# Kernel tuning notes

Measured on AMD Instinct MI355X. Metric: run time of the kernel, lower is better.

Reference implementation:

```python
import jax, jax.numpy as jnp
import numpy as np

# ---- static LSS config (matches init_kwargs) ----
B, N = 4, 6
OGFH, OGFW, DS = 256, 704, 16
FH, FW = OGFH // DS, OGFW // DS            # 16, 44
D_LO, D_HI, D_STEP = 4.0, 45.0, 1.0
D = 41                                      # len(arange(4,45,1))
CAMC = 64
NX, NY, NZ = 200, 200, 1
DX = np.array([0.5, 0.5, 20.0], np.float32)
BX = np.array([-50.0 + 0.25, -50.0 + 0.25, -10.0 + 10.0], np.float32)  # lower + dx/2


def make_frustum():
    ds = jnp.arange(D_LO, D_HI, D_STEP, dtype=jnp.float32)[:, None, None]  # (D,1,1)
    xs = jnp.linspace(0.0, OGFW - 1.0, FW, dtype=jnp.float32)[None, None, :]
    ys = jnp.linspace(0.0, OGFH - 1.0, FH, dtype=jnp.float32)[None, :, None]
    ds, ys, xs = jnp.broadcast_arrays(ds, ys, xs)
    return jnp.stack([xs, ys, ds], axis=-1)  # (D, FH, FW, 3)


def setup_inputs() -> dict:
    key = jax.random.key(0)
    k1, k2 = jax.random.split(key)
    # depthnet output (pre-softmax depth logits + context features)
    x_feats = jax.random.normal(k1, (B, N, D + CAMC, FH, FW), dtype=jnp.float32)
    # cam-to-ego rotation: camera z (depth) -> ego x, so points land in the grid
    R = np.array([[0.0, 0.0, 1.0], [-1.0, 0.0, 0.0], [0.0, -1.0, 0.0]], np.float32)
    rots = jnp.asarray(np.broadcast_to(R, (B, N, 3, 3)).copy())
    trans = jax.random.normal(k2, (B, N, 3), dtype=jnp.float32) * 0.5
    f, cx, cy = 500.0, OGFW / 2.0, OGFH / 2.0
    K = np.array([[f, 0.0, cx], [0.0, f, cy], [0.0, 0.0, 1.0]], np.float32)
    intrins = jnp.asarray(np.broadcast_to(K, (B, N, 3, 3)).copy())
    post_rots = jnp.asarray(np.broadcast_to(np.eye(3, dtype=np.float32), (B, N, 3, 3)).copy())
    post_trans = jnp.zeros((B, N, 3), dtype=jnp.float32)
    return {"x_feats": x_feats, "rots": rots, "trans": trans,
            "intrins": intrins, "post_rots": post_rots, "post_trans": post_trans}


def reference(x_feats, rots, trans, intrins, post_rots, post_trans):
    # ---- lift: depth distribution x context features ----
    depth = jax.nn.softmax(x_feats[:, :, :D], axis=2)           # (B,N,D,h,w)
    feat = x_feats[:, :, D:D + CAMC]                            # (B,N,C,h,w)
    lifted = jnp.einsum('bndhw,bnchw->bndhwc', depth, feat)     # (B,N,D,h,w,C)

    # ---- geometry: per-pixel 3D points in ego frame ----
    frustum = make_frustum()                                    # (D,h,w,3)
    pts = frustum[None, None] - post_trans[:, :, None, None, None, :]
    pts = jnp.einsum('bnij,bndhwj->bndhwi', jnp.linalg.inv(post_rots), pts)
    pts = jnp.concatenate([pts[..., :2] * pts[..., 2:3], pts[..., 2:3]], axis=-1)
    combine = rots @ jnp.linalg.inv(intrins)
    pts = jnp.einsum('bnij,bndhwj->bndhwi', combine, pts) + trans[:, :, None, None, None, :]

    # ---- voxel pooling (scatter-add == bev_pool sum) ----
    dx = jnp.asarray(DX); bx = jnp.asarray(BX)
    gidx = jnp.floor((pts - (bx - dx / 2.0)) / dx).astype(jnp.int32)  # (B,N,D,h,w,3)
    ix, iy, iz = gidx[..., 0], gidx[..., 1], gidx[..., 2]
    valid = (ix >= 0) & (ix < NX) & (iy >= 0) & (iy < NY) & (iz >= 0) & (iz < NZ)
    b_ix = jnp.arange(B, dtype=jnp.int32)[:, None, None, None, None]
    flat = ((b_ix * NZ + iz) * NX + ix) * NY + iy                # (B,N,D,h,w)
    total = B * NZ * NX * NY
    flat = jnp.where(valid, flat, total)                         # invalid -> dump bin
    out = jax.ops.segment_sum(lifted.reshape(-1, CAMC), flat.reshape(-1),
                              num_segments=total + 1)[:total]
    # (B,NZ,NX,NY,C) -> final[b, :, z, x, y], then cat z-slices along channels
    out = out.reshape(B, NZ, NX, NY, CAMC).transpose(0, 1, 4, 2, 3)
    return out.reshape(B, NZ * CAMC, NX, NY)                     # (4, 64, 200, 200)
```

## Files before the change

kernel.cpp:

```cpp
#include <hip/hip_runtime.h>
#include <math.h>

#define BB 4
#define NN 6
#define DD 41
#define CC 64
#define FHh 16
#define FWw 44
#define NXg 200
#define NYg 200
#define NZg 1
#define NPIX (BB*NN*FHh*FWw)
#define NSLOT 256
#define NOVF  (FHh*DD)
#define WSFLOATS (BB*NZg*NXg*NYg*CC)

__device__ __forceinline__ void inv3x3d(const double m[9], double o[9]) {
    double a=m[0],b=m[1],c=m[2],d=m[3],e=m[4],f=m[5],g=m[6],h=m[7],i=m[8];
    double A = e*i - f*h;
    double Bv = -(d*i - f*g);
    double Cv = d*h - e*g;
    double det = a*A + b*Bv + c*Cv;
    double r = 1.0/det;
    o[0]=A*r;  o[1]=-(b*i-c*h)*r; o[2]=(b*f-c*e)*r;
    o[3]=Bv*r; o[4]=(a*i-c*g)*r;  o[5]=-(a*f-c*d)*r;
    o[6]=Cv*r; o[7]=-(a*h-b*g)*r; o[8]=(a*e-b*d)*r;
}

__global__ __launch_bounds__(256)
void lss_zero(float4* __restrict__ p, int n4)
{
    const int stride = gridDim.x * 256;
    for (int i = blockIdx.x * 256 + threadIdx.x; i < n4; i += stride)
        p[i] = make_float4(0.f, 0.f, 0.f, 0.f);
}

__global__ __launch_bounds__(256)
void lss_scatter_dedup(const float* __restrict__ xf,
                       const float* __restrict__ rots,
                       const float* __restrict__ trans,
                       const float* __restrict__ intr,
                       const float* __restrict__ prots,
                       const float* __restrict__ ptrans,
                       float* __restrict__ ws)
{
    __shared__ int   s_keys[NSLOT];
    __shared__ float s_coef[NSLOT * FHh];
    __shared__ float s_feat[FHh * CC];
    __shared__ int2  s_ovf[NOVF];
    __shared__ float s_ovfw[NOVF];
    __shared__ int   s_ovfcnt;

    const int tid  = threadIdx.x;
    const int lane = tid & 63;
    const int wv   = tid >> 6;

    const int bid = blockIdx.x;
    const int w   = bid % FWw;
    const int rem = bid / FWw;
    const int n   = rem % NN;
    const int b   = rem / NN;
    const int cam = b*NN + n;
    const size_t pixoff = (size_t)cam * (DD+CC) * FHh * FWw + w;

    s_keys[tid] = -1;
    #pragma unroll
    for (int i = tid; i < NSLOT*FHh; i += 256) s_coef[i] = 0.0f;
    if (tid == 0) s_ovfcnt = 0;
    #pragma unroll
    for (int i = tid; i < FHh*CC; i += 256) {
        int c = i & 63, h = i >> 6;
        s_feat[i] = xf[pixoff + (size_t)(DD + c) * (FHh*FWw) + h * FWw];
    }

    double K9[9], P9[9], R9[9];
    #pragma unroll
    for (int i = 0; i < 9; ++i) {
        K9[i] = (double)intr [cam*9 + i];
        P9[i] = (double)prots[cam*9 + i];
        R9[i] = (double)rots [cam*9 + i];
    }
    double Kinv[9], Pinv[9];
    inv3x3d(K9, Kinv);
    inv3x3d(P9, Pinv);
    double M[9];
    #pragma unroll
    for (int i = 0; i < 3; ++i)
        #pragma unroll
        for (int j = 0; j < 3; ++j)
            M[i*3+j] = R9[i*3+0]*Kinv[0*3+j] + R9[i*3+1]*Kinv[1*3+j] + R9[i*3+2]*Kinv[2*3+j];
    const double tx  = (double)trans [cam*3+0], ty  = (double)trans [cam*3+1], tz  = (double)trans [cam*3+2];
    const double ptx = (double)ptrans[cam*3+0], pty = (double)ptrans[cam*3+1], ptz = (double)ptrans[cam*3+2];

    __syncthreads();

    for (int r = 0; r < 4; ++r) {
        const int h = (wv << 2) + r;
        float logit = (lane < DD)
            ? xf[pixoff + (size_t)lane * (FHh*FWw) + h * FWw] : -INFINITY;
        float mx = logit;
        #pragma unroll
        for (int off = 32; off; off >>= 1) mx = fmaxf(mx, __shfl_xor(mx, off));
        float ex = (lane < DD) ? expf(logit - mx) : 0.0f;
        float sm = ex;
        #pragma unroll
        for (int off = 32; off; off >>= 1) sm += __shfl_xor(sm, off);
        const float wgt = ex / sm;

        int seg = -1;
        if (lane < DD) {
            double dz = 4.0 + (double)lane;
            double xs = (double)w * (703.0/43.0);
            double ys = (double)h * 17.0;
            double px = xs - ptx, py = ys - pty, pz = dz - ptz;
            double qx = Pinv[0]*px + Pinv[1]*py + Pinv[2]*pz;
            double qy = Pinv[3]*px + Pinv[4]*py + Pinv[5]*pz;
            double qz = Pinv[6]*px + Pinv[7]*py + Pinv[8]*pz;
            qx *= qz; qy *= qz;
            double gx = M[0]*qx + M[1]*qy + M[2]*qz + tx;
            double gy = M[3]*qx + M[4]*qy + M[5]*qz + ty;
            double gz = M[6]*qx + M[7]*qy + M[8]*qz + tz;
            double fx = floor((gx + 50.0) / 0.5);
            double fy = floor((gy + 50.0) / 0.5);
            double fz = floor((gz + 10.0) / 20.0);
            if (fx >= 0.0 && fx < (double)NXg &&
                fy >= 0.0 && fy < (double)NYg &&
                fz >= 0.0 && fz < (double)NZg) {
                int ix = (int)fx, iy = (int)fy, iz = (int)fz;
                seg = ((b*NZg + iz)*NXg + ix)*NYg + iy;
            }
        }

        if (seg >= 0) {
            unsigned slot = (((unsigned)seg * 2654435761u) >> 20) & (NSLOT-1);
            bool done = false;
            for (int probe = 0; probe < NSLOT; ++probe) {
                int prev = atomicCAS(&s_keys[slot], -1, seg);
                if (prev == -1 || prev == seg) {
                    atomicAdd(&s_coef[slot*FHh + h], wgt);
                    done = true;
                    break;
                }
                slot = (slot + 1) & (NSLOT-1);
            }
            if (!done) {
                int k = atomicAdd(&s_ovfcnt, 1);
                s_ovf[k]  = make_int2(seg, h);
                s_ovfw[k] = wgt;
            }
        }
    }

    __syncthreads();

    for (int s = wv; s < NSLOT; s += 4) {
        int key = s_keys[s];
        if (key < 0) continue;
        float acc = 0.0f;
        #pragma unroll
        for (int h = 0; h < FHh; ++h)
            acc += s_coef[s*FHh + h] * s_feat[(h << 6) + lane];
        atomicAdd(&ws[(size_t)key * CC + lane], acc);
    }
    const int novf = s_ovfcnt;
    for (int e = wv; e < novf; e += 4) {
        int seg = s_ovf[e].x, h = s_ovf[e].y;
        atomicAdd(&ws[(size_t)seg * CC + lane], s_ovfw[e] * s_feat[(h << 6) + lane]);
    }
}

__global__ __launch_bounds__(256)
void lss_scatter_direct(const float* __restrict__ xf,
                        const float* __restrict__ rots,
                        const float* __restrict__ trans,
                        const float* __restrict__ intr,
                        const float* __restrict__ prots,
                        const float* __restrict__ ptrans,
                        float* __restrict__ acc)
{
    const int wid  = blockIdx.x * 4 + (threadIdx.x >> 6);
    const int lane = threadIdx.x & 63;
    if (wid >= NPIX) return;
    int w  = wid % FWw;
    int t1 = wid / FWw;
    int h  = t1 % FHh; t1 /= FHh;
    int n  = t1 % NN;
    int b  = t1 / NN;
    const int cam = b*NN + n;

    double K9[9], P9[9], R9[9];
    #pragma unroll
    for (int i = 0; i < 9; ++i) {
        K9[i] = (double)intr [cam*9 + i];
        P9[i] = (double)prots[cam*9 + i];
        R9[i] = (double)rots [cam*9 + i];
    }
    double Kinv[9], Pinv[9];
    inv3x3d(K9, Kinv);
    inv3x3d(P9, Pinv);
    double M[9];
    #pragma unroll
    for (int i = 0; i < 3; ++i)
        #pragma unroll
        for (int j = 0; j < 3; ++j)
            M[i*3+j] = R9[i*3+0]*Kinv[0*3+j] + R9[i*3+1]*Kinv[1*3+j] + R9[i*3+2]*Kinv[2*3+j];
    const double tx  = (double)trans [cam*3+0], ty  = (double)trans [cam*3+1], tz  = (double)trans [cam*3+2];
    const double ptx = (double)ptrans[cam*3+0], pty = (double)ptrans[cam*3+1], ptz = (double)ptrans[cam*3+2];

    const size_t pixoff = (size_t)cam * (DD+CC) * FHh * FWw + (size_t)h * FWw + w;
    float logit = (lane < DD) ? xf[pixoff + (size_t)lane * (FHh*FWw)] : -INFINITY;
    float mx = logit;
    #pragma unroll
    for (int off = 32; off; off >>= 1) mx = fmaxf(mx, __shfl_xor(mx, off));
    float ex = (lane < DD) ? expf(logit - mx) : 0.0f;
    float sm = ex;
    #pragma unroll
    for (int off = 32; off; off >>= 1) sm += __shfl_xor(sm, off);
    const float wgt = ex / sm;

    int baddr = -1;
    if (lane < DD) {
        double dz = 4.0 + (double)lane;
        double xs = (double)w * (703.0/43.0);
        double ys = (double)h * 17.0;
        double px = xs - ptx, py = ys - pty, pz = dz - ptz;
        double qx = Pinv[0]*px + Pinv[1]*py + Pinv[2]*pz;
        double qy = Pinv[3]*px + Pinv[4]*py + Pinv[5]*pz;
        double qz = Pinv[6]*px + Pinv[7]*py + Pinv[8]*pz;
        qx *= qz; qy *= qz;
        double gx = M[0]*qx + M[1]*qy + M[2]*qz + tx;
        double gy = M[3]*qx + M[4]*qy + M[5]*qz + ty;
        double gz = M[6]*qx + M[7]*qy + M[8]*qz + tz;
        double fx = floor((gx + 50.0) / 0.5);
        double fy = floor((gy + 50.0) / 0.5);
        double fz = floor((gz + 10.0) / 20.0);
        if (fx >= 0.0 && fx < (double)NXg &&
            fy >= 0.0 && fy < (double)NYg &&
            fz >= 0.0 && fz < (double)NZg) {
            int ix = (int)fx, iy = (int)fy, iz = (int)fz;
            int bz = b*NZg + iz;
            baddr = bz * (CC*NXg*NYg) + ix*NYg + iy;
        }
    }

    const float f = xf[pixoff + (size_t)(DD + lane) * (FHh*FWw)];
    for (int d = 0; d < DD; ++d) {
        int   a  = __shfl(baddr, d);
        float wd = __shfl(wgt,   d);
        if (a >= 0) atomicAdd(&acc[(size_t)a + (size_t)lane * (NXg*NYg)], wd * f);
    }
}

__global__ __launch_bounds__(256)
void lss_transpose(const float* __restrict__ ws, float* __restrict__ out)
{
    __shared__ float tile[64][65];
    const int blk  = blockIdx.x;
    const int bz   = blk / 625;
    const int xy0  = (blk % 625) * 64;
    const int lane = threadIdx.x & 63;
    const int grp  = threadIdx.x >> 6;

    const float* src = ws + ((size_t)bz * 40000 + xy0) * CC;
    #pragma unroll
    for (int i = 0; i < 16; ++i) {
        int r = grp * 16 + i;
        tile[r][lane] = src[(size_t)r * CC + lane];
    }
    __syncthreads();
    float* dst = out + (size_t)bz * CC * 40000 + xy0;
    #pragma unroll
    for (int i = 0; i < 16; ++i) {
        int cRow = grp * 16 + i;
        dst[(size_t)cRow * 40000 + lane] = tile[lane][cRow];
    }
}

extern "C" void kernel_launch(void* const* d_in, const int* in_sizes, int n_in,
                              void* d_out, int out_size, void* d_ws, size_t ws_size,
                              hipStream_t stream) {
    const float* xf     = (const float*)d_in[0];
    const float* rots   = (const float*)d_in[1];
    const float* trans  = (const float*)d_in[2];
    const float* intr   = (const float*)d_in[3];
    const float* prots  = (const float*)d_in[4];
    const float* ptrans = (const float*)d_in[5];
    float* out = (float*)d_out;

    const size_t need = (size_t)WSFLOATS * sizeof(float);

    if (ws_size >= need) {
        float* ws = (float*)d_ws;
        lss_zero<<<dim3(2048), dim3(256), 0, stream>>>((float4*)ws, WSFLOATS/4);
        lss_scatter_dedup<<<dim3(BB*NN*FWw), dim3(256), 0, stream>>>(
            xf, rots, trans, intr, prots, ptrans, ws);
        lss_transpose<<<dim3(BB*NZg*625), dim3(256), 0, stream>>>(ws, out);
    } else {
        lss_zero<<<dim3(2048), dim3(256), 0, stream>>>((float4*)out, WSFLOATS/4);
        lss_scatter_direct<<<dim3((NPIX + 3) / 4), dim3(256), 0, stream>>>(
            xf, rots, trans, intr, prots, ptrans, out);
    }
}
```

Baseline: 55.44 us.

## Replace atomic scatter into zeroed workspace with per-voxel linked-list gather

The old path zeroed a full 41 MB voxel-by-channel workspace, scatter-added into it with global float atomics, then transposed it into the output. The new path has each column block record its occupied voxels and 16 per-row coefficients into a record buffer, linked per voxel through an atomicExch head array, and saves that column's features. A gather kernel then walks each voxel's list, computes the channel sums, and writes the output directly in channel-major order. This drops the large zero fill, the float atomics and the transpose pass, at the cost of pointer-chasing reads, a smaller hash table with a last-voxel shortcut, and a block-index remap.

Result: slower. 86.72 us (+56.4%).

```diff
diff --git a/kernel.cpp b/kernel.cpp
--- a/kernel.cpp
+++ b/kernel.cpp
@@ -10,10 +10,20 @@
 #define NXg 200
 #define NYg 200
 #define NZg 1
+#define NSLOT 128
+#define NOVF  (FHh*DD)
+#define XYg (NXg*NYg)
+#define NVOX (BB*NZg*NXg*NYg)
+#define NCOL (BB*NN*FWw)
 #define NPIX (BB*NN*FHh*FWw)
-#define NSLOT 256
-#define NOVF  (FHh*DD)
-#define WSFLOATS (BB*NZg*NXg*NYg*CC)
+#define MAXREC (NCOL*NOVF)
+#define RECI 20
+
+#define HEAD_OFF 0
+#define CNT_OFF  (NVOX*4)
+#define REC_OFF  (1u<<20)
+#define FT_OFF   (REC_OFF + MAXREC*RECI*4)
+#define WS_NEED  (FT_OFF + NCOL*FHh*CC*4)
 
 __device__ __forceinline__ void inv3x3d(const double m[9], double o[9]) {
     double a=m[0],b=m[1],c=m[2],d=m[3],e=m[4],f=m[5],g=m[6],h=m[7],i=m[8];
@@ -28,49 +38,51 @@
 }
 
 __global__ __launch_bounds__(256)
-void lss_zero(float4* __restrict__ p, int n4)
+void lss_build(const float* __restrict__ xf,
+               const float* __restrict__ rots,
+               const float* __restrict__ trans,
+               const float* __restrict__ intr,
+               const float* __restrict__ prots,
+               const float* __restrict__ ptrans,
+               int* __restrict__ head,
+               int* __restrict__ cnt,
+               int* __restrict__ recs,
+               float* __restrict__ fT)
 {
-    const int stride = gridDim.x * 256;
-    for (int i = blockIdx.x * 256 + threadIdx.x; i < n4; i += stride)
-        p[i] = make_float4(0.f, 0.f, 0.f, 0.f);
-}
-
-__global__ __launch_bounds__(256)
-void lss_scatter_dedup(const float* __restrict__ xf,
-                       const float* __restrict__ rots,
-                       const float* __restrict__ trans,
-                       const float* __restrict__ intr,
-                       const float* __restrict__ prots,
-                       const float* __restrict__ ptrans,
-                       float* __restrict__ ws)
-{
+    __shared__ float s_lg[FHh * FWw];
+    __shared__ float s_feat[FHh * CC];
+    __shared__ float s_coef[NSLOT * 17];
     __shared__ int   s_keys[NSLOT];
-    __shared__ float s_coef[NSLOT * FHh];
-    __shared__ float s_feat[FHh * CC];
+    __shared__ short s_list[NSLOT];
+    __shared__ int   s_nslot;
     __shared__ int2  s_ovf[NOVF];
     __shared__ float s_ovfw[NOVF];
     __shared__ int   s_ovfcnt;
+    __shared__ int   s_base;
 
     const int tid  = threadIdx.x;
     const int lane = tid & 63;
     const int wv   = tid >> 6;
 
-    const int bid = blockIdx.x;
+    const int obid = blockIdx.x;
+    const int bid  = (obid & 7) * (NCOL / 8) + (obid >> 3);
     const int w   = bid % FWw;
     const int rem = bid / FWw;
     const int n   = rem % NN;
     const int b   = rem / NN;
     const int cam = b*NN + n;
-    const size_t pixoff = (size_t)cam * (DD+CC) * FHh * FWw + w;
-
-    s_keys[tid] = -1;
-    #pragma unroll
-    for (int i = tid; i < NSLOT*FHh; i += 256) s_coef[i] = 0.0f;
-    if (tid == 0) s_ovfcnt = 0;
-    #pragma unroll
-    for (int i = tid; i < FHh*CC; i += 256) {
-        int c = i & 63, h = i >> 6;
-        s_feat[i] = xf[pixoff + (size_t)(DD + c) * (FHh*FWw) + h * FWw];
+    const float* colbase = xf + (size_t)cam * (DD+CC) * FHh * FWw + w;
+
+    if (tid < NSLOT) s_keys[tid] = -1;
+    for (int i = tid; i < NSLOT*17; i += 256) s_coef[i] = 0.0f;
+    if (tid == 0) { s_nslot = 0; s_ovfcnt = 0; }
+
+    for (int t = tid; t < (DD+CC)*FHh; t += 256) {
+        int h  = t / (DD+CC);
+        int ch = t - h*(DD+CC);
+        float v = colbase[(size_t)ch * (FHh*FWw) + h * FWw];
+        if (ch < DD) s_lg[h*FWw + ch] = v;
+        else         s_feat[(h << 6) + (ch - DD)] = v;
     }
 
     double K9[9], P9[9], R9[9];
@@ -94,10 +106,11 @@
 
     __syncthreads();
 
+    int      last_vox  = -1;
+    unsigned last_slot = 0;
     for (int r = 0; r < 4; ++r) {
         const int h = (wv << 2) + r;
-        float logit = (lane < DD)
-            ? xf[pixoff + (size_t)lane * (FHh*FWw) + h * FWw] : -INFINITY;
+        float logit = (lane < DD) ? s_lg[h*FWw + lane] : -INFINITY;
         float mx = logit;
         #pragma unroll
         for (int off = 32; off; off >>= 1) mx = fmaxf(mx, __shfl_xor(mx, off));
@@ -107,7 +120,7 @@
         for (int off = 32; off; off >>= 1) sm += __shfl_xor(sm, off);
         const float wgt = ex / sm;
 
-        int seg = -1;
+        int vox = -1;
         if (lane < DD) {
             double dz = 4.0 + (double)lane;
             double xs = (double)w * (703.0/43.0);
@@ -127,45 +140,121 @@
                 fy >= 0.0 && fy < (double)NYg &&
                 fz >= 0.0 && fz < (double)NZg) {
                 int ix = (int)fx, iy = (int)fy, iz = (int)fz;
-                seg = ((b*NZg + iz)*NXg + ix)*NYg + iy;
+                vox = ((b*NZg + iz)*NXg + ix)*NYg + iy;
             }
         }
 
-        if (seg >= 0) {
-            unsigned slot = (((unsigned)seg * 2654435761u) >> 20) & (NSLOT-1);
-            bool done = false;
-            for (int probe = 0; probe < NSLOT; ++probe) {
-                int prev = atomicCAS(&s_keys[slot], -1, seg);
-                if (prev == -1 || prev == seg) {
-                    atomicAdd(&s_coef[slot*FHh + h], wgt);
-                    done = true;
-                    break;
+        if (vox >= 0) {
+            if (vox == last_vox) {
+                atomicAdd(&s_coef[last_slot*17 + h], wgt);
+            } else {
+                unsigned slot = (((unsigned)vox * 2654435761u) >> 18) & (NSLOT-1);
+                bool done = false;
+                for (int probe = 0; probe < NSLOT; ++probe) {
+                    int prev = atomicCAS(&s_keys[slot], -1, vox);
+                    if (prev == -1) {
+                        int k = atomicAdd(&s_nslot, 1);
+                        s_list[k] = (short)slot;
+                    }
+                    if (prev == -1 || prev == vox) {
+                        atomicAdd(&s_coef[slot*17 + h], wgt);
+                        last_vox = vox; last_slot = slot;
+                        done = true;
+                        break;
+                    }
+                    slot = (slot + 1) & (NSLOT-1);
                 }
-                slot = (slot + 1) & (NSLOT-1);
+                if (!done) {
+                    int k = atomicAdd(&s_ovfcnt, 1);
+                    s_ovf[k]  = make_int2(vox, h);
+                    s_ovfw[k] = wgt;
+                    last_vox = -1;
+                }
             }
-            if (!done) {
-                int k = atomicAdd(&s_ovfcnt, 1);
-                s_ovf[k]  = make_int2(seg, h);
-                s_ovfw[k] = wgt;
-            }
         }
     }
 
     __syncthreads();
 
-    for (int s = wv; s < NSLOT; s += 4) {
-        int key = s_keys[s];
-        if (key < 0) continue;
-        float acc = 0.0f;
-        #pragma unroll
-        for (int h = 0; h < FHh; ++h)
-            acc += s_coef[s*FHh + h] * s_feat[(h << 6) + lane];
-        atomicAdd(&ws[(size_t)key * CC + lane], acc);
-    }
+    const int nocc = s_nslot;
     const int novf = s_ovfcnt;
+    if (tid == 0) s_base = atomicAdd(cnt, nocc + novf);
+    {
+        float* ft = fT + (size_t)bid * (FHh*CC);
+        for (int i = tid; i < FHh*CC; i += 256) ft[i] = s_feat[i];
+    }
+    __syncthreads();
+    const int base = s_base;
+
+    for (int e = wv; e < nocc; e += 4) {
+        int slot = s_list[e];
+        int vox  = s_keys[slot];
+        int ridx = base + e;
+        int* rec = recs + (size_t)ridx * RECI;
+        if (lane >= 32 && lane < 48)
+            ((float*)rec)[4 + (lane-32)] = s_coef[slot*17 + (lane-32)];
+        if (lane == 0) {
+            rec[0] = vox;
+            rec[2] = bid;
+            rec[1] = atomicExch(&head[vox], ridx);
+        }
+    }
     for (int e = wv; e < novf; e += 4) {
-        int seg = s_ovf[e].x, h = s_ovf[e].y;
-        atomicAdd(&ws[(size_t)seg * CC + lane], s_ovfw[e] * s_feat[(h << 6) + lane]);
+        int vox = s_ovf[e].x, h = s_ovf[e].y;
+        int ridx = base + nocc + e;
+        int* rec = recs + (size_t)ridx * RECI;
+        if (lane >= 32 && lane < 48)
+            ((float*)rec)[4 + (lane-32)] = ((lane-32) == h) ? s_ovfw[e] : 0.0f;
+        if (lane == 0) {
+            rec[0] = vox;
+            rec[2] = bid;
+            rec[1] = atomicExch(&head[vox], ridx);
+        }
+    }
+}
+
+__global__ __launch_bounds__(256)
+void lss_gather(const int* __restrict__ head,
+                const int* __restrict__ recs,
+                const float* __restrict__ fT,
+                float* __restrict__ out)
+{
+    __shared__ float s_acc[CC * 65];
+    const int blk  = blockIdx.x;
+    const int bz   = blk / 625;
+    const int xy0  = (blk % 625) * 64;
+    const int tid  = threadIdx.x;
+    const int lane = tid & 63;
+    const int wv   = tid >> 6;
+
+    for (int cell = wv; cell < 64; cell += 4) {
+        const int vox = bz * XYg + xy0 + cell;
+        float a = 0.0f;
+        int ptr = head[vox];
+        while (ptr >= 0) {
+            const int* rec = recs + (size_t)ptr * RECI;
+            const int col  = rec[2];
+            const float4* cp = (const float4*)(rec + 4);
+            float4 c0 = cp[0], c1 = cp[1], c2 = cp[2], c3 = cp[3];
+            const float* fb = fT + (size_t)col * (FHh*CC) + lane;
+            a += c0.x*fb[0*64]  + c0.y*fb[1*64]  + c0.z*fb[2*64]  + c0.w*fb[3*64]
+               + c1.x*fb[4*64]  + c1.y*fb[5*64]  + c1.z*fb[6*64]  + c1.w*fb[7*64]
+               + c2.x*fb[8*64]  + c2.y*fb[9*64]  + c2.z*fb[10*64] + c2.w*fb[11*64]
+               + c3.x*fb[12*64] + c3.y*fb[13*64] + c3.z*fb[14*64] + c3.w*fb[15*64];
+            ptr = rec[1];
+        }
+        s_acc[lane*65 + cell] = a;
+    }
+    __syncthreads();
+
+    float* dst = out + (size_t)bz * CC * XYg + xy0;
+    #pragma unroll
+    for (int rep = 0; rep < 4; ++rep) {
+        int c = (wv << 4) + (rep << 2) + (lane >> 4);
+        int q = lane & 15;
+        float4 v = make_float4(s_acc[c*65 + 4*q + 0], s_acc[c*65 + 4*q + 1],
+                               s_acc[c*65 + 4*q + 2], s_acc[c*65 + 4*q + 3]);
+        ((float4*)(dst + (size_t)c * XYg))[q] = v;
     }
 }
 
@@ -239,7 +328,7 @@
             fz >= 0.0 && fz < (double)NZg) {
             int ix = (int)fx, iy = (int)fy, iz = (int)fz;
             int bz = b*NZg + iz;
-            baddr = bz * (CC*NXg*NYg) + ix*NYg + iy;
+            baddr = bz * (CC*XYg) + ix*NYg + iy;
         }
     }
 
@@ -247,33 +336,16 @@
     for (int d = 0; d < DD; ++d) {
         int   a  = __shfl(baddr, d);
         float wd = __shfl(wgt,   d);
-        if (a >= 0) atomicAdd(&acc[(size_t)a + (size_t)lane * (NXg*NYg)], wd * f);
+        if (a >= 0) atomicAdd(&acc[(size_t)a + (size_t)lane * XYg], wd * f);
     }
 }
 
 __global__ __launch_bounds__(256)
-void lss_transpose(const float* __restrict__ ws, float* __restrict__ out)
+void lss_zero(float4* __restrict__ p, int n4)
 {
-    __shared__ float tile[64][65];
-    const int blk  = blockIdx.x;
-    const int bz   = blk / 625;
-    const int xy0  = (blk % 625) * 64;
-    const int lane = threadIdx.x & 63;
-    const int grp  = threadIdx.x >> 6;
-
-    const float* src = ws + ((size_t)bz * 40000 + xy0) * CC;
-    #pragma unroll
-    for (int i = 0; i < 16; ++i) {
-        int r = grp * 16 + i;
-        tile[r][lane] = src[(size_t)r * CC + lane];
-    }
-    __syncthreads();
-    float* dst = out + (size_t)bz * CC * 40000 + xy0;
-    #pragma unroll
-    for (int i = 0; i < 16; ++i) {
-        int cRow = grp * 16 + i;
-        dst[(size_t)cRow * 40000 + lane] = tile[lane][cRow];
-    }
+    const int stride = gridDim.x * 256;
+    for (int i = blockIdx.x * 256 + threadIdx.x; i < n4; i += stride)
+        p[i] = make_float4(0.f, 0.f, 0.f, 0.f);
 }
 
 extern "C" void kernel_launch(void* const* d_in, const int* in_sizes, int n_in,
@@ -287,16 +359,20 @@
     const float* ptrans = (const float*)d_in[5];
     float* out = (float*)d_out;
 
-    const size_t need = (size_t)WSFLOATS * sizeof(float);
-
-    if (ws_size >= need) {
-        float* ws = (float*)d_ws;
-        lss_zero<<<dim3(2048), dim3(256), 0, stream>>>((float4*)ws, WSFLOATS/4);
-        lss_scatter_dedup<<<dim3(BB*NN*FWw), dim3(256), 0, stream>>>(
-            xf, rots, trans, intr, prots, ptrans, ws);
-        lss_transpose<<<dim3(BB*NZg*625), dim3(256), 0, stream>>>(ws, out);
+    if (ws_size >= (size_t)WS_NEED) {
+        char* wsb = (char*)d_ws;
+        int*   head = (int*)(wsb + HEAD_OFF);
+        int*   cnt  = (int*)(wsb + CNT_OFF);
+        int*   recs = (int*)(wsb + REC_OFF);
+        float* fT   = (float*)(wsb + FT_OFF);
+        hipMemsetAsync(head, 0xFF, (size_t)NVOX * sizeof(int), stream);
+        hipMemsetAsync(cnt, 0, sizeof(int), stream);
+        lss_build<<<dim3(NCOL), dim3(256), 0, stream>>>(
+            xf, rots, trans, intr, prots, ptrans, head, cnt, recs, fT);
+        lss_gather<<<dim3(BB*NZg*625), dim3(256), 0, stream>>>(head, recs, fT, out);
     } else {
-        lss_zero<<<dim3(2048), dim3(256), 0, stream>>>((float4*)out, WSFLOATS/4);
+        lss_zero<<<dim3(2048), dim3(256), 0, stream>>>(
+            (float4*)out, (BB*NZg*XYg*CC)/4);
         lss_scatter_direct<<<dim3((NPIX + 3) / 4), dim3(256), 0, stream>>>(
             xf, rots, trans, intr, prots, ptrans, out);
     }
```
